# Kernel tuning notes

Hardware: AMD Instinct MI355X
Metric: run time of the kernel (lower is better)

## Reference

```python
import jax, jax.numpy as jnp
import numpy as np
import math

HEADS = 2
DH = 64
INNER = HEADS * DH  # 128
TOPK = 128
ALPHA = 10.0
N_FREQ = 8  # feature_dim // (2*input_dim) = 64 // 8
OMEGAS = jnp.logspace(1.0, math.log10(128.0), N_FREQ)           # sigma_q = 128
OMEGAS_L = [jnp.logspace(1.0, math.log10(s), N_FREQ) for s in (128.0, 32.0)]
LAYER_NUM = 2


def calc_gamma(grid, omegas):
    # grid: (Q, 4) -> (Q, 4*2*n_freq)
    arg = jnp.pi * grid[:, :, None] * omegas[None, None, :]      # (Q,4,n)
    g = jnp.concatenate([jnp.sin(arg), jnp.cos(arg)], axis=-1)   # (Q,4,2n)
    return g.reshape(grid.shape[0], -1)


def setup_inputs() -> dict:
    key = jax.random.key(0)
    ks = jax.random.split(key, 20)
    B, Q, L, HD, FD, OD = 2, 4096, 1024, 256, 64, 1

    def w(k, shape, fan_in):
        return jax.random.normal(k, shape, dtype=jnp.float32) * (1.0 / np.sqrt(fan_in))

    inp = {
        'x': jax.random.uniform(ks[0], (B, Q, 4), dtype=jnp.float32),
        'tokens': jax.random.normal(ks[1], (B, L, HD), dtype=jnp.float32),
        'query_W': w(ks[2], (FD, HD), FD),
        'query_b': jnp.zeros((HD,), jnp.float32),
        'q_W': w(ks[3], (HD, INNER), HD),
        'kv_W': w(ks[4], (HD, 2 * INNER), HD),
        'out_W': w(ks[5], (INNER, HD), INNER),
        'out_b': jnp.zeros((HD,), jnp.float32),
        'band_W': w(ks[6], (LAYER_NUM, FD, HD), FD),
        'band_b': jnp.zeros((LAYER_NUM, HD), jnp.float32),
        'mod_W': w(ks[7], (LAYER_NUM, HD, HD), HD),
        'mod_b': jnp.zeros((LAYER_NUM, HD), jnp.float32),
        'hv_W': w(ks[8], (LAYER_NUM - 1, HD, HD), HD),
        'hv_b': jnp.zeros((LAYER_NUM - 1, HD), jnp.float32),
        'outl_W': w(ks[9], (LAYER_NUM, HD, OD), HD),
        'outl_b': jnp.zeros((LAYER_NUM, OD), jnp.float32),
        'gD': 8, 'gH': 8, 'gW': 8, 'gT': 8,
    }
    return inp


def reference(x, tokens, query_W, query_b, q_W, kv_W, out_W, out_b,
              band_W, band_b, mod_W, mod_b, hv_W, hv_b, outl_W, outl_b,
              gD, gH, gW, gT):
    B, Q, _ = x.shape
    L = tokens.shape[1]
    grid = x[0]  # (Q, 4) — torch code uses x[0] for all batches

    # --- patch index + approximate relative distances -> sparse attn indices ---
    z_i = (grid[:, 0] * gD).astype(jnp.int32)
    y_i = (grid[:, 1] * gH).astype(jnp.int32)
    x_i = (grid[:, 2] * gW).astype(jnp.int32)
    t_i = (grid[:, 3] * gT).astype(jnp.int32)
    idx = ((t_i * gD + z_i) * gH + y_i) * gW + x_i               # (Q,)
    N = gD * gH * gW * gT
    t = idx / N                                                  # (Q,) float
    tok_pos = (jnp.arange(L, dtype=jnp.float32) + 0.5) / L       # (L,)
    bias = ALPHA * (t[:, None] - tok_pos[None, :]) ** 2          # (Q, L)
    # top-k SMALLEST distances (identical across batch, compute once)
    _, attn_idx = jax.lax.top_k(-bias, TOPK)                     # (Q, k)

    # --- query features ---
    gamma_q = calc_gamma(grid, OMEGAS)                           # (Q, 64)
    x_q = jax.nn.relu(gamma_q @ query_W + query_b)               # (Q, 256)
    x_q = jnp.broadcast_to(x_q[None], (B, Q, x_q.shape[-1]))

    # --- sparse shared-token cross attention ---
    scale = DH ** -0.5
    q = (x_q @ q_W).reshape(B, Q, HEADS, DH)                     # (B,Q,H,Dh)
    kv = tokens @ kv_W                                           # (B,L,2*inner)
    k_full, v_full = kv[..., :INNER], kv[..., INNER:]            # (B,L,inner)
    k_sp = k_full[:, attn_idx, :].reshape(B, Q, TOPK, HEADS, DH)  # (B,Q,k,H,Dh)
    v_sp = v_full[:, attn_idx, :].reshape(B, Q, TOPK, HEADS, DH)
    sim = jnp.einsum('bqhd,bqkhd->bhqk', q, k_sp) * scale        # (B,H,Q,k)
    attn = jax.nn.softmax(sim, axis=-1)
    o = jnp.einsum('bhqk,bqkhd->bqhd', attn, v_sp).reshape(B, Q, INNER)
    modulation = o @ out_W + out_b                               # (B,Q,256)

    # --- per-band modulation ---
    mods = []
    for l in range(LAYER_NUM):
        gamma_l = calc_gamma(grid, OMEGAS_L[l])                  # (Q, 64)
        h_l = jax.nn.relu(gamma_l @ band_W[l] + band_b[l])       # (Q, 256)
        m_l = jax.nn.relu(h_l[None] + modulation @ mod_W[l] + mod_b[l])
        mods.append(m_l)

    h_v = [mods[0]]
    for i in range(LAYER_NUM - 1):
        h_v.append(jax.nn.relu((mods[i + 1] + h_v[i]) @ hv_W[i] + hv_b[i]))

    out = sum(h_v[i] @ outl_W[i] + outl_b[i] for i in range(LAYER_NUM))
    return out  # (B, Q, output_dim)
```

## Files before the change

### kernel.cpp

```cpp
#include <hip/hip_runtime.h>
#include <math.h>

#define BN     2
#define QN     4096
#define LN     1024
#define TOPKN  128
#define PI_F   3.14159265358979323846f

#define K_OM0  0.3642064529893673
#define K_OM1  0.1661644014008115

#define NCMAX  320
#define PFP    328

typedef __attribute__((ext_vector_type(8))) short  s16x8;
typedef __attribute__((ext_vector_type(4))) short  s16x4;
typedef __attribute__((ext_vector_type(4))) float  f32x4;
typedef unsigned short u16;

__device__ __forceinline__ u16 f2bf(float f) {
    unsigned int u = __float_as_uint(f);
    u = (u + 0x7FFFu + ((u >> 16) & 1u)) >> 16;
    return (u16)u;
}

struct KvS { u16 tok[32 * 264]; u16 stage[256 * 40]; float vtile[128][40]; };
struct QS  { float shx[128]; u16 gam[32 * 72]; u16 xq[32 * 264]; u16 stage[256 * 40]; };
struct TrS { float tile[32][33]; };
struct SoS { int hist[1024]; int cur[1024]; };
union PrepS { KvS kv; QS q; TrS tr; SoS so; };

__global__ __launch_bounds__(1024) void prep_kernel(
    const float* __restrict__ tokens, const float* __restrict__ kv_W,
    const float* __restrict__ x, const float* __restrict__ query_W,
    const float* __restrict__ query_b, const float* __restrict__ q_W,
    const float* __restrict__ outW, const float* __restrict__ bandW,
    const float* __restrict__ modW, const float* __restrict__ hvW,
    const int* __restrict__ gDp, const int* __restrict__ gHp,
    const int* __restrict__ gWp, const int* __restrict__ gTp,
    float* __restrict__ qall, u16* __restrict__ kbf, u16* __restrict__ vtbf,
    u16* __restrict__ outT, u16* __restrict__ bandT,
    u16* __restrict__ modT, u16* __restrict__ hvT,
    int* __restrict__ perm, int* __restrict__ ssort)
{
    __shared__ __align__(16) PrepS sm;
    const int bid = blockIdx.x;
    const int t   = threadIdx.x;
    const int wid = t >> 6, lane = t & 63;
    const int quad = lane >> 4, l16 = lane & 15;

    if (bid < 64) {
        int l0 = bid * 32;
        int b = l0 >> 10, lloc = l0 & 1023;
        #pragma unroll
        for (int i = 0; i < 8; i++) {
            int idx = i * 1024 + t; int row = idx >> 8, col = idx & 255;
            sm.kv.tok[row * 264 + col] = f2bf(tokens[(size_t)(l0 + row) * 256 + col]);
        }
        int m0 = (wid & 1) * 16;
        int c0 = (wid >> 1) * 32;
        f32x4 acc[2];
        acc[0] = (f32x4){0.f, 0.f, 0.f, 0.f};
        acc[1] = (f32x4){0.f, 0.f, 0.f, 0.f};
        for (int kc = 0; kc < 8; kc++) {
            __syncthreads();
            #pragma unroll
            for (int i = 0; i < 8; i++) {
                int idx = i * 1024 + t; int k = idx >> 8, n = idx & 255;
                sm.kv.stage[n * 40 + k] = f2bf(kv_W[(size_t)(kc * 32 + k) * 256 + n]);
            }
            __syncthreads();
            s16x8 a = *(const s16x8*)&sm.kv.tok[(m0 + l16) * 264 + kc * 32 + quad * 8];
            #pragma unroll
            for (int sub = 0; sub < 2; sub++) {
                s16x8 bfr = *(const s16x8*)&sm.kv.stage[(c0 + sub * 16 + l16) * 40 + quad * 8];
                acc[sub] = __builtin_amdgcn_mfma_f32_16x16x32_bf16(a, bfr, acc[sub], 0, 0, 0);
            }
        }
        #pragma unroll
        for (int sub = 0; sub < 2; sub++) {
            int col = c0 + sub * 16 + l16;
            if (col < 128) {
                #pragma unroll
                for (int r = 0; r < 4; r++)
                    kbf[(size_t)(l0 + m0 + quad * 4 + r) * 128 + col] = f2bf(acc[sub][r]);
            } else {
                #pragma unroll
                for (int r = 0; r < 4; r++)
                    sm.kv.vtile[col - 128][m0 + quad * 4 + r] = acc[sub][r];
            }
        }
        __syncthreads();
        {
            int col = t >> 3, rg = (t & 7) * 4;
            float4 v4 = *(const float4*)&sm.kv.vtile[col][rg];
            s16x4 pk;
            pk[0] = (short)f2bf(v4.x); pk[1] = (short)f2bf(v4.y);
            pk[2] = (short)f2bf(v4.z); pk[3] = (short)f2bf(v4.w);
            *(s16x4*)&vtbf[(size_t)(b * 128 + col) * 1024 + lloc + rg] = pk;
        }
    } else if (bid < 192) {
        int p0 = (bid - 64) * 32;
        if (t < 128) sm.q.shx[t] = x[p0 * 4 + t];
        __syncthreads();
        #pragma unroll
        for (int j = 0; j < 2; j++) {
            int e = t * 2 + j;
            int g = e >> 6, f = e & 63;
            int c = f >> 4, jj = f & 15, oi = jj & 7;
            float om = (float)(10.0 * exp((double)oi * K_OM0));
            float arg = PI_F * sm.q.shx[g * 4 + c] * om;
            sm.q.gam[g * 72 + f] = f2bf((jj < 8) ? sinf(arg) : cosf(arg));
        }
        int m0 = (wid & 1) * 16;
        {
            int c0 = (wid >> 1) * 32;
            f32x4 acc[2];
            acc[0] = (f32x4){0.f, 0.f, 0.f, 0.f};
            acc[1] = (f32x4){0.f, 0.f, 0.f, 0.f};
            for (int kc = 0; kc < 2; kc++) {
                __syncthreads();
                #pragma unroll
                for (int i = 0; i < 8; i++) {
                    int idx = i * 1024 + t; int k = idx >> 8, n = idx & 255;
                    sm.q.stage[n * 40 + k] = f2bf(query_W[(size_t)(kc * 32 + k) * 256 + n]);
                }
                __syncthreads();
                s16x8 a = *(const s16x8*)&sm.q.gam[(m0 + l16) * 72 + kc * 32 + quad * 8];
                #pragma unroll
                for (int sub = 0; sub < 2; sub++) {
                    s16x8 bfr = *(const s16x8*)&sm.q.stage[(c0 + sub * 16 + l16) * 40 + quad * 8];
                    acc[sub] = __builtin_amdgcn_mfma_f32_16x16x32_bf16(a, bfr, acc[sub], 0, 0, 0);
                }
            }
            #pragma unroll
            for (int sub = 0; sub < 2; sub++) {
                int col = c0 + sub * 16 + l16;
                float bias = query_b[col];
                #pragma unroll
                for (int r = 0; r < 4; r++)
                    sm.q.xq[(m0 + quad * 4 + r) * 264 + col] = f2bf(fmaxf(acc[sub][r] + bias, 0.f));
            }
        }
        {
            int n0q = (wid >> 1) * 16;
            f32x4 acc2 = (f32x4){0.f, 0.f, 0.f, 0.f};
            for (int kc = 0; kc < 8; kc++) {
                __syncthreads();
                #pragma unroll
                for (int i = 0; i < 4; i++) {
                    int idx = i * 1024 + t; int k = idx >> 7, n = idx & 127;
                    sm.q.stage[n * 40 + k] = f2bf(q_W[(size_t)(kc * 32 + k) * 128 + n]);
                }
                __syncthreads();
                s16x8 a = *(const s16x8*)&sm.q.xq[(m0 + l16) * 264 + kc * 32 + quad * 8];
                s16x8 bfr = *(const s16x8*)&sm.q.stage[(n0q + l16) * 40 + quad * 8];
                acc2 = __builtin_amdgcn_mfma_f32_16x16x32_bf16(a, bfr, acc2, 0, 0, 0);
            }
            #pragma unroll
            for (int r = 0; r < 4; r++)
                qall[(size_t)(p0 + m0 + quad * 4 + r) * 128 + n0q + l16] = acc2[r];
        }
    } else if (bid < 448) {
        int bid2 = bid - 192;
        const float* src; u16* dst; int K, N, lt;
        if      (bid2 < 32)  { src = outW;  dst = outT;  K = 128; N = 256; lt = bid2; }
        else if (bid2 < 64)  { src = bandW; dst = bandT; K = 128; N = 256; lt = bid2 - 32; }
        else if (bid2 < 192) { src = modW;  dst = modT;  K = 512; N = 256; lt = bid2 - 64; }
        else                 { src = hvW;   dst = hvT;   K = 256; N = 256; lt = bid2 - 192; }
        int tk = K >> 5;
        int ktile = lt % tk, nt = lt / tk;
        int k0 = ktile * 32, n0 = nt * 32;
        int tx = t & 31, ty = (t >> 5) & 31;
        sm.tr.tile[ty][tx] = src[(size_t)(k0 + ty) * N + n0 + tx];
        __syncthreads();
        dst[(size_t)(n0 + ty) * K + k0 + tx] = f2bf(sm.tr.tile[tx][ty]);
    } else {
        int gD = gDp[0], gH = gHp[0], gW = gWp[0], gT = gTp[0];
        int Ng = gD * gH * gW * gT;
        sm.so.hist[t] = 0;
        __syncthreads();
        int sarr[4];
        #pragma unroll
        for (int i = 0; i < 4; i++) {
            int q = i * 1024 + t;
            float4 xv = *(const float4*)&x[q * 4];
            int zi = (int)(xv.x * (float)gD);
            int yi = (int)(xv.y * (float)gH);
            int xi = (int)(xv.z * (float)gW);
            int ti = (int)(xv.w * (float)gT);
            int idx = ((ti * gD + zi) * gH + yi) * gW + xi;
            float tt = (float)idx / (float)Ng;
            int s = (int)ceilf(tt * (float)LN - ((float)(TOPKN / 2) + 0.5f));
            s = min(max(s, 0), LN - TOPKN);
            sarr[i] = s;
            atomicAdd(&sm.so.hist[s], 1);
        }
        __syncthreads();
        int cnt = sm.so.hist[t];
        sm.so.cur[t] = cnt;
        __syncthreads();
        for (int off = 1; off < 1024; off <<= 1) {
            int u = (t >= off) ? sm.so.cur[t - off] : 0;
            __syncthreads();
            sm.so.cur[t] += u;
            __syncthreads();
        }
        int excl = sm.so.cur[t] - cnt;
        __syncthreads();
        sm.so.hist[t] = excl;
        __syncthreads();
        #pragma unroll
        for (int i = 0; i < 4; i++) {
            int q = i * 1024 + t;
            int pos = atomicAdd(&sm.so.hist[sarr[i]], 1);
            perm[pos] = q;
            ssort[pos] = sarr[i];
        }
    }
}

__global__ __launch_bounds__(1024, 8) void fused_kernel(
    const float* __restrict__ x,
    const u16* __restrict__ kbf, const u16* __restrict__ vtbf,
    const float* __restrict__ qall,
    const int* __restrict__ perm, const int* __restrict__ ssort,
    const u16* __restrict__ outT, const float* __restrict__ out_b,
    const u16* __restrict__ bandT, const float* __restrict__ band_b,
    const u16* __restrict__ modT, const float* __restrict__ mod_b,
    const u16* __restrict__ hvT, const float* __restrict__ hv_b,
    const float* __restrict__ outl_W, const float* __restrict__ outl_b,
    float* __restrict__ out)
{
    const int bid = blockIdx.x;
    const int b   = bid >> 8;
    const int sp0 = (bid & 255) * 16;
    const int t   = threadIdx.x;
    const int wid = t >> 6, lane = t & 63;
    const int quad = lane >> 4, l16 = lane & 15;

    __shared__ __align__(16) u16 q_bf[16 * 136];
    __shared__ __align__(16) u16 gam_lds[32 * 72];
    __shared__ __align__(16) u16 P_bf[32 * PFP];
    __shared__ __align__(16) unsigned char regionA[PFP * 16 * 4];
    __shared__ __align__(16) u16 o_lds[16 * 136];
    __shared__ float fin[256];
    __shared__ float sh_xc[64];
    __shared__ int sh_pq[16], sh_s[16];

    float* P_f32 = (float*)regionA;
    float* o_part = (float*)regionA;
    u16* modu_lds = (u16*)regionA;
    u16* s01_lds  = (u16*)(regionA + 16 * 264 * 2);

    if (t < 16) { sh_pq[t] = perm[sp0 + t]; sh_s[t] = ssort[sp0 + t]; }
    __syncthreads();

    {
        int m = t >> 6, d = (t & 63) * 2;
        float2 qv = *(const float2*)&qall[(size_t)sh_pq[m] * 128 + d];
        unsigned int pk = (unsigned int)f2bf(qv.x) | ((unsigned int)f2bf(qv.y) << 16);
        *(unsigned int*)&q_bf[m * 136 + d] = pk;
    }
    if (t < 64) sh_xc[t] = x[(size_t)sh_pq[t >> 2] * 4 + (t & 3)];
    __syncthreads();

    #pragma unroll
    for (int j = 0; j < 2; j++) {
        int e = t * 2 + j;
        int l = e >> 10, g = (e >> 6) & 15, f = e & 63;
        int c = f >> 4, jj = f & 15, oi = jj & 7;
        float om = (float)(10.0 * exp((double)oi * (l ? K_OM1 : K_OM0)));
        float arg = PI_F * sh_xc[g * 4 + c] * om;
        gam_lds[(l * 16 + g) * 72 + f] = f2bf((jj < 8) ? sinf(arg) : cosf(arg));
    }

    const int u0    = sh_s[0] & ~7;
    const int ncols = min((sh_s[15] + 128 - u0 + 31) & ~31, NCMAX);
    const int nsub  = ncols >> 4;
    const int nkc   = ncols >> 5;

    #pragma unroll
    for (int h = 0; h < 2; h++) {
        s16x8 aq0 = *(const s16x8*)&q_bf[l16 * 136 + h * 64 + quad * 8];
        s16x8 aq1 = *(const s16x8*)&q_bf[l16 * 136 + h * 64 + 32 + quad * 8];
        for (int sub = wid; sub < nsub; sub += 16) {
            f32x4 acc = (f32x4){0.f, 0.f, 0.f, 0.f};
            size_t krow = (size_t)(b * 1024 + u0 + sub * 16 + l16) * 128 + h * 64 + quad * 8;
            s16x8 b0 = *(const s16x8*)&kbf[krow];
            s16x8 b1 = *(const s16x8*)&kbf[krow + 32];
            acc = __builtin_amdgcn_mfma_f32_16x16x32_bf16(aq0, b0, acc, 0, 0, 0);
            acc = __builtin_amdgcn_mfma_f32_16x16x32_bf16(aq1, b1, acc, 0, 0, 0);
            #pragma unroll
            for (int r = 0; r < 4; r++)
                P_f32[(quad * 4 + r) * PFP + sub * 16 + l16] = acc[r];
        }
        __syncthreads();
        {
            int g = wid;
            int sg = sh_s[g];
            float vals[5]; int ok[5];
            float mx = -1e30f;
            #pragma unroll
            for (int i = 0; i < 5; i++) {
                int c = lane + 64 * i;
                float v = P_f32[g * PFP + c] * 0.125f;
                int key = u0 + c;
                int o2 = (c < ncols) && (key >= sg) && (key < sg + 128);
                vals[i] = v; ok[i] = o2;
                if (o2) mx = fmaxf(mx, v);
            }
            #pragma unroll
            for (int off = 1; off < 64; off <<= 1) mx = fmaxf(mx, __shfl_xor(mx, off));
            float sum = 0.f, e5[5];
            #pragma unroll
            for (int i = 0; i < 5; i++) {
                float e = ok[i] ? expf(vals[i] - mx) : 0.f;
                e5[i] = e; sum += e;
            }
            #pragma unroll
            for (int off = 1; off < 64; off <<= 1) sum += __shfl_xor(sum, off);
            float inv = 1.f / sum;
            #pragma unroll
            for (int i = 0; i < 5; i++) {
                int c = lane + 64 * i;
                if (c < ncols) P_bf[(h * 16 + g) * PFP + c] = f2bf(e5[i] * inv);
            }
        }
        __syncthreads();
    }

    {
        int n0 = (wid & 7) * 16;
        int hh = n0 >> 6;
        int khalf = wid >> 3;
        int nk2 = (nkc + 1) >> 1;
        int k0 = khalf ? nk2 : 0;
        int k1 = khalf ? nkc : nk2;
        f32x4 acc = (f32x4){0.f, 0.f, 0.f, 0.f};
        for (int kc = k0; kc < k1; kc++) {
            s16x8 a = *(const s16x8*)&P_bf[(hh * 16 + l16) * PFP + kc * 32 + quad * 8];
            int koff = u0 + kc * 32 + quad * 8;
            koff = min(koff, 1016);
            s16x8 bfr = *(const s16x8*)&vtbf[(size_t)(b * 128 + n0 + l16) * 1024 + koff];
            acc = __builtin_amdgcn_mfma_f32_16x16x32_bf16(a, bfr, acc, 0, 0, 0);
        }
        #pragma unroll
        for (int r = 0; r < 4; r++)
            o_part[(khalf * 16 + quad * 4 + r) * 128 + n0 + l16] = acc[r];
    }
    __syncthreads();

    {
        int m = t >> 6, j2 = (t & 63) * 2;
        float v0 = o_part[m * 128 + j2]     + o_part[(16 + m) * 128 + j2];
        float v1 = o_part[m * 128 + j2 + 1] + o_part[(16 + m) * 128 + j2 + 1];
        unsigned int pk = (unsigned int)f2bf(v0) | ((unsigned int)f2bf(v1) << 16);
        *(unsigned int*)&o_lds[m * 136 + j2] = pk;
    }
    __syncthreads();

    const int n0 = wid * 16;
    float m0f[4];

    {
        f32x4 acc = (f32x4){0.f, 0.f, 0.f, 0.f};
        #pragma unroll
        for (int kc = 0; kc < 4; kc++) {
            s16x8 a = *(const s16x8*)&o_lds[l16 * 136 + kc * 32 + quad * 8];
            s16x8 bfr = *(const s16x8*)&outT[(size_t)(n0 + l16) * 128 + kc * 32 + quad * 8];
            acc = __builtin_amdgcn_mfma_f32_16x16x32_bf16(a, bfr, acc, 0, 0, 0);
        }
        int col = n0 + l16;
        float bias = out_b[col];
        #pragma unroll
        for (int r = 0; r < 4; r++)
            modu_lds[(quad * 4 + r) * 264 + col] = f2bf(acc[r] + bias);
    }
    __syncthreads();

    #pragma unroll
    for (int l = 0; l < 2; l++) {
        f32x4 acc1 = (f32x4){0.f, 0.f, 0.f, 0.f};
        f32x4 acc2 = (f32x4){0.f, 0.f, 0.f, 0.f};
        #pragma unroll
        for (int kc = 0; kc < 2; kc++) {
            s16x8 a = *(const s16x8*)&gam_lds[(l * 16 + l16) * 72 + kc * 32 + quad * 8];
            s16x8 bfr = *(const s16x8*)&bandT[(size_t)(n0 + l16) * 128 + l * 64 + kc * 32 + quad * 8];
            acc1 = __builtin_amdgcn_mfma_f32_16x16x32_bf16(a, bfr, acc1, 0, 0, 0);
        }
        #pragma unroll
        for (int kc = 0; kc < 8; kc++) {
            s16x8 a = *(const s16x8*)&modu_lds[l16 * 264 + kc * 32 + quad * 8];
            s16x8 bfr = *(const s16x8*)&modT[(size_t)(n0 + l16) * 512 + l * 256 + kc * 32 + quad * 8];
            acc2 = __builtin_amdgcn_mfma_f32_16x16x32_bf16(a, bfr, acc2, 0, 0, 0);
        }
        int col = n0 + l16;
        float bb = band_b[l * 256 + col];
        float mb = mod_b[l * 256 + col];
        #pragma unroll
        for (int r = 0; r < 4; r++) {
            float hval = fmaxf(acc1[r] + bb, 0.f);
            float mval = fmaxf(hval + acc2[r] + mb, 0.f);
            if (l == 0) m0f[r] = mval;
            else s01_lds[(quad * 4 + r) * 264 + col] = f2bf(m0f[r] + mval);
        }
    }
    __syncthreads();

    {
        f32x4 acc = (f32x4){0.f, 0.f, 0.f, 0.f};
        #pragma unroll
        for (int kc = 0; kc < 8; kc++) {
            s16x8 a = *(const s16x8*)&s01_lds[l16 * 264 + kc * 32 + quad * 8];
            s16x8 bfr = *(const s16x8*)&hvT[(size_t)(n0 + l16) * 256 + kc * 32 + quad * 8];
            acc = __builtin_amdgcn_mfma_f32_16x16x32_bf16(a, bfr, acc, 0, 0, 0);
        }
        int col = n0 + l16;
        float w0 = outl_W[col], w1 = outl_W[256 + col], hb = hv_b[col];
        #pragma unroll
        for (int r = 0; r < 4; r++) {
            float hvv = fmaxf(acc[r] + hb, 0.f);
            float pv = m0f[r] * w0 + hvv * w1;
            #pragma unroll
            for (int off = 1; off < 16; off <<= 1) pv += __shfl_xor(pv, off);
            if (l16 == 0) fin[wid * 16 + quad * 4 + r] = pv;
        }
    }
    __syncthreads();
    if (t < 16) {
        float s2 = outl_b[0] + outl_b[1];
        #pragma unroll
        for (int w = 0; w < 16; w++) s2 += fin[w * 16 + t];
        out[(size_t)b * QN + sh_pq[t]] = s2;
    }
}

extern "C" void kernel_launch(void* const* d_in, const int* in_sizes, int n_in,
                              void* d_out, int out_size, void* d_ws, size_t ws_size,
                              hipStream_t stream)
{
    const float* x       = (const float*)d_in[0];
    const float* tokens  = (const float*)d_in[1];
    const float* query_W = (const float*)d_in[2];
    const float* query_b = (const float*)d_in[3];
    const float* q_W     = (const float*)d_in[4];
    const float* kv_W    = (const float*)d_in[5];
    const float* out_W   = (const float*)d_in[6];
    const float* out_b   = (const float*)d_in[7];
    const float* band_W  = (const float*)d_in[8];
    const float* band_b  = (const float*)d_in[9];
    const float* mod_W   = (const float*)d_in[10];
    const float* mod_b   = (const float*)d_in[11];
    const float* hv_W    = (const float*)d_in[12];
    const float* hv_b    = (const float*)d_in[13];
    const float* outl_W  = (const float*)d_in[14];
    const float* outl_b  = (const float*)d_in[15];
    const int*   gD      = (const int*)d_in[16];
    const int*   gH      = (const int*)d_in[17];
    const int*   gW      = (const int*)d_in[18];
    const int*   gT      = (const int*)d_in[19];

    float* ws   = (float*)d_ws;
    float* qall = ws;
    u16* wb = (u16*)(ws + 524288);
    u16* kbf   = wb;
    u16* vtbf  = wb + 262144;
    u16* outT  = wb + 524288;
    u16* bandT = wb + 557056;
    u16* modT  = wb + 589824;
    u16* hvT   = wb + 720896;
    int* perm  = (int*)(wb + 786432);
    int* ssort = perm + 4096;
    float* out = (float*)d_out;

    prep_kernel<<<449, 1024, 0, stream>>>(tokens, kv_W, x, query_W, query_b, q_W,
                                          out_W, band_W, mod_W, hv_W,
                                          gD, gH, gW, gT,
                                          qall, kbf, vtbf, outT, bandT, modT, hvT,
                                          perm, ssort);
    fused_kernel<<<512, 1024, 0, stream>>>(x, kbf, vtbf, qall, perm, ssort,
        outT, out_b, bandT, band_b, modT, mod_b, hvT, hv_b,
        outl_W, outl_b, out);
}
```

Baseline: 145.8 us.

## Store K, V and weight matrices in MFMA-fragment tiled layouts for coalesced loads

The prep kernel now writes the bf16 K, transposed V and transposed weight matrices in blocked layouts that match the 16x32 MFMA fragment access pattern, so each wavefront's operand loads hit contiguous 1KB chunks instead of strided rows. The attention start column alignment changes from 8 to 16 so K tiles line up with the 16-row blocks. This is meant to cut global-memory transaction count in the main kernel, at the cost of scattered small writes in the prep kernel and extra index arithmetic.

Result: faster. 130.0 us (-10.8%).

```diff
diff --git a/kernel.cpp b/kernel.cpp
--- a/kernel.cpp
+++ b/kernel.cpp
@@ -22,6 +22,16 @@
     unsigned int u = __float_as_uint(f);
     u = (u + 0x7FFFu + ((u >> 16) & 1u)) >> 16;
     return (u16)u;
+}
+
+__device__ __forceinline__ size_t wtile(int n, int k, int K) {
+    return (size_t)((n >> 4) * (K >> 5) + (k >> 5)) * 512 + (n & 15) * 32 + (k & 31);
+}
+__device__ __forceinline__ size_t kidx(int b, int l, int d) {
+    return (((size_t)(b * 64 + (l >> 4)) * 16 + (d >> 3)) * 16 + (l & 15)) * 8 + (d & 7);
+}
+__device__ __forceinline__ size_t vidx(int b, int n, int k) {
+    return (((size_t)(b * 8 + (n >> 4)) * 128 + (k >> 3)) * 16 + (n & 15)) * 8 + (k & 7);
 }
 
 struct KvS { u16 tok[32 * 264]; u16 stage[256 * 40]; float vtile[128][40]; };
@@ -82,8 +92,10 @@
             int col = c0 + sub * 16 + l16;
             if (col < 128) {
                 #pragma unroll
-                for (int r = 0; r < 4; r++)
-                    kbf[(size_t)(l0 + m0 + quad * 4 + r) * 128 + col] = f2bf(acc[sub][r]);
+                for (int r = 0; r < 4; r++) {
+                    int lg = l0 + m0 + quad * 4 + r;
+                    kbf[kidx(lg >> 10, lg & 1023, col)] = f2bf(acc[sub][r]);
+                }
             } else {
                 #pragma unroll
                 for (int r = 0; r < 4; r++)
@@ -97,7 +109,7 @@
             s16x4 pk;
             pk[0] = (short)f2bf(v4.x); pk[1] = (short)f2bf(v4.y);
             pk[2] = (short)f2bf(v4.z); pk[3] = (short)f2bf(v4.w);
-            *(s16x4*)&vtbf[(size_t)(b * 128 + col) * 1024 + lloc + rg] = pk;
+            *(s16x4*)&vtbf[vidx(b, col, lloc + rg)] = pk;
         }
     } else if (bid < 192) {
         int p0 = (bid - 64) * 32;
@@ -174,7 +186,7 @@
         int tx = t & 31, ty = (t >> 5) & 31;
         sm.tr.tile[ty][tx] = src[(size_t)(k0 + ty) * N + n0 + tx];
         __syncthreads();
-        dst[(size_t)(n0 + ty) * K + k0 + tx] = f2bf(sm.tr.tile[tx][ty]);
+        dst[wtile(n0 + ty, k0 + tx, K)] = f2bf(sm.tr.tile[tx][ty]);
     } else {
         int gD = gDp[0], gH = gHp[0], gW = gWp[0], gT = gTp[0];
         int Ng = gD * gH * gW * gT;
@@ -275,7 +287,7 @@
         gam_lds[(l * 16 + g) * 72 + f] = f2bf((jj < 8) ? sinf(arg) : cosf(arg));
     }
 
-    const int u0    = sh_s[0] & ~7;
+    const int u0    = sh_s[0] & ~15;
     const int ncols = min((sh_s[15] + 128 - u0 + 31) & ~31, NCMAX);
     const int nsub  = ncols >> 4;
     const int nkc   = ncols >> 5;
@@ -286,9 +298,9 @@
         s16x8 aq1 = *(const s16x8*)&q_bf[l16 * 136 + h * 64 + 32 + quad * 8];
         for (int sub = wid; sub < nsub; sub += 16) {
             f32x4 acc = (f32x4){0.f, 0.f, 0.f, 0.f};
-            size_t krow = (size_t)(b * 1024 + u0 + sub * 16 + l16) * 128 + h * 64 + quad * 8;
-            s16x8 b0 = *(const s16x8*)&kbf[krow];
-            s16x8 b1 = *(const s16x8*)&kbf[krow + 32];
+            int lrow = u0 + sub * 16 + l16;
+            s16x8 b0 = *(const s16x8*)&kbf[kidx(b, lrow, h * 64 + quad * 8)];
+            s16x8 b1 = *(const s16x8*)&kbf[kidx(b, lrow, h * 64 + 32 + quad * 8)];
             acc = __builtin_amdgcn_mfma_f32_16x16x32_bf16(aq0, b0, acc, 0, 0, 0);
             acc = __builtin_amdgcn_mfma_f32_16x16x32_bf16(aq1, b1, acc, 0, 0, 0);
             #pragma unroll
@@ -342,7 +354,7 @@
             s16x8 a = *(const s16x8*)&P_bf[(hh * 16 + l16) * PFP + kc * 32 + quad * 8];
             int koff = u0 + kc * 32 + quad * 8;
             koff = min(koff, 1016);
-            s16x8 bfr = *(const s16x8*)&vtbf[(size_t)(b * 128 + n0 + l16) * 1024 + koff];
+            s16x8 bfr = *(const s16x8*)&vtbf[vidx(b, n0 + l16, koff)];
             acc = __builtin_amdgcn_mfma_f32_16x16x32_bf16(a, bfr, acc, 0, 0, 0);
         }
         #pragma unroll
@@ -368,7 +380,7 @@
         #pragma unroll
         for (int kc = 0; kc < 4; kc++) {
             s16x8 a = *(const s16x8*)&o_lds[l16 * 136 + kc * 32 + quad * 8];
-            s16x8 bfr = *(const s16x8*)&outT[(size_t)(n0 + l16) * 128 + kc * 32 + quad * 8];
+            s16x8 bfr = *(const s16x8*)&outT[wtile(n0 + l16, kc * 32 + quad * 8, 128)];
             acc = __builtin_amdgcn_mfma_f32_16x16x32_bf16(a, bfr, acc, 0, 0, 0);
         }
         int col = n0 + l16;
@@ -386,13 +398,13 @@
         #pragma unroll
         for (int kc = 0; kc < 2; kc++) {
             s16x8 a = *(const s16x8*)&gam_lds[(l * 16 + l16) * 72 + kc * 32 + quad * 8];
-            s16x8 bfr = *(const s16x8*)&bandT[(size_t)(n0 + l16) * 128 + l * 64 + kc * 32 + quad * 8];
+            s16x8 bfr = *(const s16x8*)&bandT[wtile(n0 + l16, l * 64 + kc * 32 + quad * 8, 128)];
             acc1 = __builtin_amdgcn_mfma_f32_16x16x32_bf16(a, bfr, acc1, 0, 0, 0);
         }
         #pragma unroll
         for (int kc = 0; kc < 8; kc++) {
             s16x8 a = *(const s16x8*)&modu_lds[l16 * 264 + kc * 32 + quad * 8];
-            s16x8 bfr = *(const s16x8*)&modT[(size_t)(n0 + l16) * 512 + l * 256 + kc * 32 + quad * 8];
+            s16x8 bfr = *(const s16x8*)&modT[wtile(n0 + l16, l * 256 + kc * 32 + quad * 8, 512)];
             acc2 = __builtin_amdgcn_mfma_f32_16x16x32_bf16(a, bfr, acc2, 0, 0, 0);
         }
         int col = n0 + l16;
@@ -413,7 +425,7 @@
         #pragma unroll
         for (int kc = 0; kc < 8; kc++) {
             s16x8 a = *(const s16x8*)&s01_lds[l16 * 264 + kc * 32 + quad * 8];
-            s16x8 bfr = *(const s16x8*)&hvT[(size_t)(n0 + l16) * 256 + kc * 32 + quad * 8];
+            s16x8 bfr = *(const s16x8*)&hvT[wtile(n0 + l16, kc * 32 + quad * 8, 256)];
             acc = __builtin_amdgcn_mfma_f32_16x16x32_bf16(a, bfr, acc, 0, 0, 0);
         }
         int col = n0 + l16;
```
